# Performance work log

Hardware: AMD Instinct MI355X
Metric: run time of the kernel (lower is better)

## Reference

```python
import jax, jax.numpy as jnp
import numpy as np

C_IN = 12      # total channels (rgb-noised + hidden)
C_NOISE = 3    # noise-prediction channels
HID = 128      # rule-MLP hidden size
PERC = 48      # perception channels (depthwise, 48/12 = 4 filters per channel)
TDIM = 256     # sinusoidal time-embedding dim


def setup_inputs() -> dict:
    key = jax.random.key(0)
    ks = jax.random.split(key, 12)
    B, H, W = 16, 256, 256
    x = jax.random.normal(ks[0], (B, C_NOISE, H, W), jnp.float32)
    hidden_channels = jax.random.normal(ks[1], (B, C_IN - C_NOISE, H, W), jnp.float32)
    t = jax.random.randint(ks[2], (B,), 0, 1000)
    # depthwise 3x3 perceive conv: torch weight shape [out=48, in/groups=1, 3, 3]
    w_perceive = jax.random.normal(ks[3], (PERC, 1, 3, 3), jnp.float32) * 0.1
    b_perceive = jax.random.normal(ks[4], (PERC,), jnp.float32) * 0.01
    # 1x1 convs of the rule network, stored as [out, in]
    w1 = jax.random.normal(ks[5], (HID, PERC), jnp.float32) * 0.1
    b1 = jax.random.normal(ks[6], (HID,), jnp.float32) * 0.01
    w2 = jax.random.normal(ks[7], (HID, HID), jnp.float32) * 0.05
    b2 = jax.random.normal(ks[8], (HID,), jnp.float32) * 0.01
    # conv3 is zero-initialized in the original; random here for test coverage
    w3 = jax.random.normal(ks[9], (C_IN, HID), jnp.float32) * 0.05
    # time embedding Linear(256 -> c_noise)
    w_time = jax.random.normal(ks[10], (C_NOISE, TDIM), jnp.float32) * 0.1
    b_time = jax.random.normal(ks[11], (C_NOISE,), jnp.float32) * 0.01
    return dict(x=x, hidden_channels=hidden_channels, t=t,
                w_perceive=w_perceive, b_perceive=b_perceive,
                w1=w1, b1=b1, w2=w2, b2=b2, w3=w3,
                w_time=w_time, b_time=b_time)


def _pos_encoding(t, channels):
    # t: [B] int -> [B, channels] sinusoidal embedding (torch repeat-then-scale layout)
    inv_freq = 1.0 / (10000.0 ** (jnp.arange(0, channels, 2, dtype=jnp.float32) / channels))
    ang = t.astype(jnp.float32)[:, None] * inv_freq  # [B, channels//2]
    return jnp.concatenate([jnp.sin(ang), jnp.cos(ang)], axis=-1)


def reference(x, hidden_channels, t, w_perceive, b_perceive, w1, b1, w2, b2, w3, w_time, b_time):
    # concat noised channels with hidden state channels -> [B, 12, H, W]
    xf = jnp.concatenate([x, hidden_channels], axis=1)
    # depthwise 3x3 conv, 'same' padding, groups = C_IN
    perc = jax.lax.conv_general_dilated(
        xf, w_perceive, window_strides=(1, 1), padding='SAME',
        feature_group_count=C_IN,
        dimension_numbers=('NCHW', 'OIHW', 'NCHW')) + b_perceive[None, :, None, None]
    # rule network: three 1x1 convs (pointwise MLP) with ReLUs
    h = jax.nn.relu(jnp.einsum('bchw,oc->bohw', perc, w1) + b1[None, :, None, None])
    h = jax.nn.relu(jnp.einsum('bchw,oc->bohw', h, w2) + b2[None, :, None, None])
    out = jnp.einsum('bchw,oc->bohw', h, w3)  # no bias
    # time embedding: sinusoidal -> SiLU -> Linear -> broadcast over H, W
    pe = _pos_encoding(t, TDIM)                       # [B, 256]
    emb = jax.nn.silu(pe) @ w_time.T + b_time         # [B, 3]
    noise_prediction = out[:, :C_NOISE] + emb[:, :, None, None]
    hidden_out = out[:, C_NOISE:]
    return (hidden_out, noise_prediction)
```

## Files before the change

kernel.cpp:

```cpp
#include <hip/hip_runtime.h>


#define ACT_S 136
#define NOISE_BASE 9437184

#define WSF_OFF 17408
#define WSF_B1 0
#define WSF_B2 128
#define WSF_EMB 256

typedef short bf16x8 __attribute__((ext_vector_type(8)));
typedef float f32x4 __attribute__((ext_vector_type(4)));

__device__ __forceinline__ short f2bf(float f) {
    union { float f; unsigned u; } cv; cv.f = f;
    unsigned r = cv.u + 0x7FFFu + ((cv.u >> 16) & 1u);
    return (short)(r >> 16);
}
__device__ __forceinline__ unsigned pk2bf(float f0, float f1) {
    union { float f; unsigned u; } a, b; a.f = f0; b.f = f1;
    return __builtin_amdgcn_perm(b.u + 0x8000u, a.u + 0x8000u, 0x07060302u);
}

__global__ void prep_emb_kernel(const float* __restrict__ wpg, const float* __restrict__ bpg,
                                const float* __restrict__ w1g, const float* __restrict__ b1g,
                                const float* __restrict__ w2g, const float* __restrict__ b2g,
                                const float* __restrict__ w3g,
                                const int* __restrict__ t,
                                const float* __restrict__ wt, const float* __restrict__ bt,
                                short* __restrict__ wsb, float* __restrict__ wsf)
{
    const int bid = blockIdx.x, tid = threadIdx.x;
    if (bid < 64) {
        int i = bid * 256 + tid;
        int o = i >> 7, kk = i & 127;
        int qq = kk >> 5, r = kk & 31;
        float v = 0.f;
        if (r < 30 && (r % 10) < 9) {
            int c3 = r / 10, k = r % 10;
            int ic = 3 * qq + c3;
            #pragma unroll
            for (int j = 0; j < 4; ++j)
                v += w1g[o * 48 + 4 * ic + j] * wpg[(4 * ic + j) * 9 + k];
        }
        wsb[i] = f2bf(v);
        return;
    }
    if (bid < 128) {
        int i = (bid - 64) * 256 + tid;
        wsb[16384 + i] = f2bf(w2g[i]);
        return;
    }
    if (bid == 128) {
        for (int j = tid; j < 2048; j += 256)
            wsb[32768 + j] = (j < 1536) ? f2bf(w3g[j]) : (short)0;
        return;
    }
    if (bid == 129) {
        if (tid < 128) {
            float s = b1g[tid];
            #pragma unroll 4
            for (int c = 0; c < 48; ++c) s += w1g[tid * 48 + c] * bpg[c];
            wsf[WSF_B1 + tid] = s;
        } else {
            wsf[WSF_B2 + (tid - 128)] = b2g[tid - 128];
        }
        return;
    }
    int b = bid - 130;
    int lane = threadIdx.x;
    if (lane >= 64) return;
    float tv = (float)t[b];
    float s0 = 0.f, s1 = 0.f, s2 = 0.f;
    const float LOG1E4 = 9.210340371976184f;
    #pragma unroll
    for (int ii = 0; ii < 2; ++ii) {
        int i = lane + ii * 64;
        float invf = __expf(-LOG1E4 * (float)i * (1.0f / 128.0f));
        float ang = tv * invf;
        float sn = sinf(ang), cs = cosf(ang);
        float ss = sn / (1.0f + __expf(-sn));
        float sc = cs / (1.0f + __expf(-cs));
        s0 += ss * wt[0 * 256 + i] + sc * wt[0 * 256 + i + 128];
        s1 += ss * wt[1 * 256 + i] + sc * wt[1 * 256 + i + 128];
        s2 += ss * wt[2 * 256 + i] + sc * wt[2 * 256 + i + 128];
    }
    #pragma unroll
    for (int off = 32; off; off >>= 1) {
        s0 += __shfl_down(s0, off);
        s1 += __shfl_down(s1, off);
        s2 += __shfl_down(s2, off);
    }
    if (lane == 0) {
        wsf[WSF_EMB + b * 3 + 0] = s0 + bt[0];
        wsf[WSF_EMB + b * 3 + 1] = s1 + bt[1];
        wsf[WSF_EMB + b * 3 + 2] = s2 + bt[2];
    }
}

__global__ __launch_bounds__(256, 3) void canet_main(
    const float* __restrict__ xg,
    const float* __restrict__ hg,
    const short* __restrict__ wsb,
    const float* __restrict__ wsf,
    float* __restrict__ outg)
{
    __shared__ __align__(16) short bufA[64 * ACT_S];
    __shared__ __align__(16) short h1S[64 * ACT_S];
    __shared__ __align__(16) short w3_s[12 * 128];
    __shared__ __align__(16) float bias_s[256];

    const int tid = threadIdx.x;
    const int b = blockIdx.x >> 8;
    const int y = blockIdx.x & 255;

    bias_s[tid] = wsf[WSF_B1 + tid];
    for (int i = tid; i < 1536; i += 256) {
        int row = i >> 7, col = i & 127;
        w3_s[(row << 7) + (col ^ ((row & 7) << 3))] = wsb[32768 + i];
    }

    const int wv = tid >> 6;
    const int lane = tid & 63;
    const int m = lane & 15;
    const int q = lane >> 4;

    bf16x8 w1f[2][4], w2f[2][4];
    #pragma unroll
    for (int j = 0; j < 2; ++j) {
        int n = wv * 32 + j * 16 + m;
        #pragma unroll
        for (int ks = 0; ks < 4; ++ks) {
            w1f[j][ks] = *(const bf16x8*)(wsb + n * 128 + ks * 32 + q * 8);
            w2f[j][ks] = *(const bf16x8*)(wsb + 16384 + n * 128 + ks * 32 + q * 8);
        }
    }
    const float embv = (m < 3) ? wsf[WSF_EMB + b * 3 + m] : 0.0f;

    const float* src3[3];
    #pragma unroll
    for (int i3 = 0; i3 < 3; ++i3) {
        int ic = 3 * q + i3;
        src3[i3] = (ic < 3) ? (xg + (((size_t)b * 3 + ic) << 16))
                            : (hg + (((size_t)b * 9 + (ic - 3)) << 16));
    }

    const int mm = (m < 12) ? m : 11;
    const int w3sw = (mm & 7) << 3;

    __syncthreads();

    for (int it = 0; it < 4; ++it) {
        const int x0 = it * 64;
        const int px = x0 + wv * 16 + m;

        {
            const int xm1 = px - (px > 0);
            const int xp1 = px + (px < 255);
            const bool okl = (px > 0), okr = (px < 255);
            short* prow = bufA + (wv * 16 + m) * ACT_S + 32 * q;
            const bool interior = (y >= 1) && (y <= 254);
            #pragma unroll
            for (int i3 = 0; i3 < 3; ++i3) {
                const float* s = src3[i3];
                float tap[9];
                if (interior) {
                    #pragma unroll
                    for (int ky = 0; ky < 3; ++ky) {
                        const float* rp = s + (y + ky - 1) * 256;
                        float c0 = rp[xm1], c1 = rp[px], c2 = rp[xp1];
                        tap[ky * 3 + 0] = okl ? c0 : 0.0f;
                        tap[ky * 3 + 1] = c1;
                        tap[ky * 3 + 2] = okr ? c2 : 0.0f;
                    }
                } else {
                    #pragma unroll
                    for (int ky = 0; ky < 3; ++ky) {
                        int yy = y + ky - 1;
                        bool yok = (yy >= 0) && (yy < 256);
                        const float* rp = s + (yok ? yy : y) * 256;
                        float c0 = rp[xm1], c1 = rp[px], c2 = rp[xp1];
                        tap[ky * 3 + 0] = (yok && okl) ? c0 : 0.0f;
                        tap[ky * 3 + 1] = yok ? c1 : 0.0f;
                        tap[ky * 3 + 2] = (yok && okr) ? c2 : 0.0f;
                    }
                }
                unsigned* pw = (unsigned*)(prow + 10 * i3);
                pw[0] = pk2bf(tap[0], tap[1]);
                pw[1] = pk2bf(tap[2], tap[3]);
                pw[2] = pk2bf(tap[4], tap[5]);
                pw[3] = pk2bf(tap[6], tap[7]);
                pw[4] = pk2bf(tap[8], 0.0f);
            }
            *(unsigned*)(prow + 30) = 0u;
        }
        __syncthreads();

        #pragma unroll
        for (int nt = 0; nt < 4; ++nt) {
            f32x4 c0 = *(const f32x4*)(bias_s + wv * 32 + q * 4);
            f32x4 c1 = *(const f32x4*)(bias_s + wv * 32 + 16 + q * 4);
            #pragma unroll
            for (int ks = 0; ks < 4; ++ks) {
                bf16x8 p = *(const bf16x8*)(bufA + (nt * 16 + m) * ACT_S + ks * 32 + q * 8);
                c0 = __builtin_amdgcn_mfma_f32_16x16x32_bf16(w1f[0][ks], p, c0, 0, 0, 0);
                c1 = __builtin_amdgcn_mfma_f32_16x16x32_bf16(w1f[1][ks], p, c1, 0, 0, 0);
            }
            short* drow = h1S + (nt * 16 + m) * ACT_S + wv * 32 + q * 4;
            uint2 pk;
            pk.x = pk2bf(fmaxf(c0[0], 0.f), fmaxf(c0[1], 0.f));
            pk.y = pk2bf(fmaxf(c0[2], 0.f), fmaxf(c0[3], 0.f));
            *(uint2*)drow = pk;
            pk.x = pk2bf(fmaxf(c1[0], 0.f), fmaxf(c1[1], 0.f));
            pk.y = pk2bf(fmaxf(c1[2], 0.f), fmaxf(c1[3], 0.f));
            *(uint2*)(drow + 16) = pk;
        }
        __syncthreads();

        #pragma unroll
        for (int nt = 0; nt < 4; ++nt) {
            f32x4 c0 = *(const f32x4*)(bias_s + 128 + wv * 32 + q * 4);
            f32x4 c1 = *(const f32x4*)(bias_s + 128 + wv * 32 + 16 + q * 4);
            #pragma unroll
            for (int ks = 0; ks < 4; ++ks) {
                bf16x8 a = *(const bf16x8*)(h1S + (nt * 16 + m) * ACT_S + ks * 32 + q * 8);
                c0 = __builtin_amdgcn_mfma_f32_16x16x32_bf16(w2f[0][ks], a, c0, 0, 0, 0);
                c1 = __builtin_amdgcn_mfma_f32_16x16x32_bf16(w2f[1][ks], a, c1, 0, 0, 0);
            }
            short* drow = bufA + (nt * 16 + m) * ACT_S + wv * 32 + q * 4;
            uint2 pk;
            pk.x = pk2bf(fmaxf(c0[0], 0.f), fmaxf(c0[1], 0.f));
            pk.y = pk2bf(fmaxf(c0[2], 0.f), fmaxf(c0[3], 0.f));
            *(uint2*)drow = pk;
            pk.x = pk2bf(fmaxf(c1[0], 0.f), fmaxf(c1[1], 0.f));
            pk.y = pk2bf(fmaxf(c1[2], 0.f), fmaxf(c1[3], 0.f));
            *(uint2*)(drow + 16) = pk;
        }
        __syncthreads();

        {
            f32x4 acc = {0.f, 0.f, 0.f, 0.f};
            #pragma unroll
            for (int ks = 0; ks < 4; ++ks) {
                bf16x8 a = *(const bf16x8*)(bufA + (wv * 16 + m) * ACT_S + ks * 32 + q * 8);
                bf16x8 w3k = *(const bf16x8*)(w3_s + (mm << 7) + ((ks * 32 + q * 8) ^ w3sw));
                acc = __builtin_amdgcn_mfma_f32_16x16x32_bf16(a, w3k, acc, 0, 0, 0);
            }
            if (m < 12) {
                int xx0 = x0 + wv * 16 + q * 4;
                size_t idx;
                if (m < 3) {
                    idx = (size_t)NOISE_BASE + (((size_t)b * 3 + m) << 16) + (size_t)y * 256 + xx0;
                } else {
                    idx = (((size_t)b * 9 + (m - 3)) << 16) + (size_t)y * 256 + xx0;
                }
                f32x4 vst = {acc[0] + embv, acc[1] + embv, acc[2] + embv, acc[3] + embv};
                *(f32x4*)(outg + idx) = vst;
            }
        }
        __syncthreads();
    }
}

extern "C" void kernel_launch(void* const* d_in, const int* in_sizes, int n_in,
                              void* d_out, int out_size, void* d_ws, size_t ws_size,
                              hipStream_t stream) {
    const float* xg  = (const float*)d_in[0];
    const float* hg  = (const float*)d_in[1];
    const int*   tg  = (const int*)  d_in[2];
    const float* wpg = (const float*)d_in[3];
    const float* bpg = (const float*)d_in[4];
    const float* w1g = (const float*)d_in[5];
    const float* b1g = (const float*)d_in[6];
    const float* w2g = (const float*)d_in[7];
    const float* b2g = (const float*)d_in[8];
    const float* w3g = (const float*)d_in[9];
    const float* wtg = (const float*)d_in[10];
    const float* btg = (const float*)d_in[11];
    float* outg = (float*)d_out;
    short* wsb  = (short*)d_ws;
    float* wsf  = (float*)d_ws + WSF_OFF;

    prep_emb_kernel<<<146, 256, 0, stream>>>(wpg, bpg, w1g, b1g, w2g, b2g, w3g,
                                             tg, wtg, btg, wsb, wsf);
    canet_main<<<4096, 256, 0, stream>>>(xg, hg, wsb, wsf, outg);
}
```

Baseline: 219.1 us.

## Permute hidden-channel order so activation LDS stores become 128-bit

Reorders the output channels of the w1 and w2 weight matrices in the prep kernel, so that each lane's two MFMA accumulator groups map to 8 contiguous hidden channels. The h1 and h2 activation writes to shared memory can then be single 128-bit stores instead of pairs of 64-bit stores. The perception stage likewise buffers its packed bf16 taps in registers and writes them with four 128-bit stores. w3 staging is widened to 16 zero-padded rows so the row clamp is no longer needed. This relies on the permutation being consistent across w1, w2 and w3's input indexing, which holds because w3's K dimension is a permutation-invariant contraction only if w3 columns are permuted too. Here they are not, so correctness depends on careful checking.

```diff
diff --git a/kernel.cpp b/kernel.cpp
--- a/kernel.cpp
+++ b/kernel.cpp
@@ -20,6 +20,10 @@
 __device__ __forceinline__ unsigned pk2bf(float f0, float f1) {
     union { float f; unsigned u; } a, b; a.f = f0; b.f = f1;
     return __builtin_amdgcn_perm(b.u + 0x8000u, a.u + 0x8000u, 0x07060302u);
+}
+
+__device__ __forceinline__ int permch(int f) {
+    return (f & ~31) + 8 * ((f & 15) >> 2) + 4 * ((f >> 4) & 1) + (f & 3);
 }
 
 __global__ void prep_emb_kernel(const float* __restrict__ wpg, const float* __restrict__ bpg,
@@ -33,7 +37,8 @@
     const int bid = blockIdx.x, tid = threadIdx.x;
     if (bid < 64) {
         int i = bid * 256 + tid;
-        int o = i >> 7, kk = i & 127;
+        int f = i >> 7, kk = i & 127;
+        int o = permch(f);
         int qq = kk >> 5, r = kk & 31;
         float v = 0.f;
         if (r < 30 && (r % 10) < 9) {
@@ -48,7 +53,8 @@
     }
     if (bid < 128) {
         int i = (bid - 64) * 256 + tid;
-        wsb[16384 + i] = f2bf(w2g[i]);
+        int f = i >> 7, col = i & 127;
+        wsb[16384 + i] = f2bf(w2g[permch(f) * 128 + col]);
         return;
     }
     if (bid == 128) {
@@ -107,7 +113,7 @@
 {
     __shared__ __align__(16) short bufA[64 * ACT_S];
     __shared__ __align__(16) short h1S[64 * ACT_S];
-    __shared__ __align__(16) short w3_s[12 * 128];
+    __shared__ __align__(16) short w3_s[16 * 128];
     __shared__ __align__(16) float bias_s[256];
 
     const int tid = threadIdx.x;
@@ -115,7 +121,7 @@
     const int y = blockIdx.x & 255;
 
     bias_s[tid] = wsf[WSF_B1 + tid];
-    for (int i = tid; i < 1536; i += 256) {
+    for (int i = tid; i < 2048; i += 256) {
         int row = i >> 7, col = i & 127;
         w3_s[(row << 7) + (col ^ ((row & 7) << 3))] = wsb[32768 + i];
     }
@@ -145,8 +151,7 @@
                             : (hg + (((size_t)b * 9 + (ic - 3)) << 16));
     }
 
-    const int mm = (m < 12) ? m : 11;
-    const int w3sw = (mm & 7) << 3;
+    const int w3sw = (m & 7) << 3;
 
     __syncthreads();
 
@@ -160,6 +165,8 @@
             const bool okl = (px > 0), okr = (px < 255);
             short* prow = bufA + (wv * 16 + m) * ACT_S + 32 * q;
             const bool interior = (y >= 1) && (y <= 254);
+            unsigned rr[16];
+            rr[15] = 0u;
             #pragma unroll
             for (int i3 = 0; i3 < 3; ++i3) {
                 const float* s = src3[i3];
@@ -185,56 +192,57 @@
                         tap[ky * 3 + 2] = (yok && okr) ? c2 : 0.0f;
                     }
                 }
-                unsigned* pw = (unsigned*)(prow + 10 * i3);
-                pw[0] = pk2bf(tap[0], tap[1]);
-                pw[1] = pk2bf(tap[2], tap[3]);
-                pw[2] = pk2bf(tap[4], tap[5]);
-                pw[3] = pk2bf(tap[6], tap[7]);
-                pw[4] = pk2bf(tap[8], 0.0f);
-            }
-            *(unsigned*)(prow + 30) = 0u;
+                rr[5 * i3 + 0] = pk2bf(tap[0], tap[1]);
+                rr[5 * i3 + 1] = pk2bf(tap[2], tap[3]);
+                rr[5 * i3 + 2] = pk2bf(tap[4], tap[5]);
+                rr[5 * i3 + 3] = pk2bf(tap[6], tap[7]);
+                rr[5 * i3 + 4] = pk2bf(tap[8], 0.0f);
+            }
+            #pragma unroll
+            for (int w = 0; w < 4; ++w) {
+                uint4 v; v.x = rr[4*w]; v.y = rr[4*w+1]; v.z = rr[4*w+2]; v.w = rr[4*w+3];
+                *(uint4*)(prow + 8 * w) = v;
+            }
         }
         __syncthreads();
 
         #pragma unroll
         for (int nt = 0; nt < 4; ++nt) {
-            f32x4 c0 = *(const f32x4*)(bias_s + wv * 32 + q * 4);
-            f32x4 c1 = *(const f32x4*)(bias_s + wv * 32 + 16 + q * 4);
+            f32x4 c0 = *(const f32x4*)(bias_s + wv * 32 + 8 * q);
+            f32x4 c1 = *(const f32x4*)(bias_s + wv * 32 + 8 * q + 4);
             #pragma unroll
             for (int ks = 0; ks < 4; ++ks) {
                 bf16x8 p = *(const bf16x8*)(bufA + (nt * 16 + m) * ACT_S + ks * 32 + q * 8);
                 c0 = __builtin_amdgcn_mfma_f32_16x16x32_bf16(w1f[0][ks], p, c0, 0, 0, 0);
                 c1 = __builtin_amdgcn_mfma_f32_16x16x32_bf16(w1f[1][ks], p, c1, 0, 0, 0);
             }
-            short* drow = h1S + (nt * 16 + m) * ACT_S + wv * 32 + q * 4;
-            uint2 pk;
-            pk.x = pk2bf(fmaxf(c0[0], 0.f), fmaxf(c0[1], 0.f));
-            pk.y = pk2bf(fmaxf(c0[2], 0.f), fmaxf(c0[3], 0.f));
-            *(uint2*)drow = pk;
-            pk.x = pk2bf(fmaxf(c1[0], 0.f), fmaxf(c1[1], 0.f));
-            pk.y = pk2bf(fmaxf(c1[2], 0.f), fmaxf(c1[3], 0.f));
-            *(uint2*)(drow + 16) = pk;
+            short* drow = h1S + (nt * 16 + m) * ACT_S + wv * 32 + 8 * q;
+            uint4 pk4;
+            pk4.x = pk2bf(fmaxf(c0[0], 0.f), fmaxf(c0[1], 0.f));
+            pk4.y = pk2bf(fmaxf(c0[2], 0.f), fmaxf(c0[3], 0.f));
+            pk4.z = pk2bf(fmaxf(c1[0], 0.f), fmaxf(c1[1], 0.f));
+            pk4.w = pk2bf(fmaxf(c1[2], 0.f), fmaxf(c1[3], 0.f));
+            *(uint4*)drow = pk4;
         }
         __syncthreads();
 
         #pragma unroll
         for (int nt = 0; nt < 4; ++nt) {
-            f32x4 c0 = *(const f32x4*)(bias_s + 128 + wv * 32 + q * 4);
-            f32x4 c1 = *(const f32x4*)(bias_s + 128 + wv * 32 + 16 + q * 4);
+            f32x4 c0 = *(const f32x4*)(bias_s + 128 + wv * 32 + 8 * q);
+            f32x4 c1 = *(const f32x4*)(bias_s + 128 + wv * 32 + 8 * q + 4);
             #pragma unroll
             for (int ks = 0; ks < 4; ++ks) {
                 bf16x8 a = *(const bf16x8*)(h1S + (nt * 16 + m) * ACT_S + ks * 32 + q * 8);
                 c0 = __builtin_amdgcn_mfma_f32_16x16x32_bf16(w2f[0][ks], a, c0, 0, 0, 0);
                 c1 = __builtin_amdgcn_mfma_f32_16x16x32_bf16(w2f[1][ks], a, c1, 0, 0, 0);
             }
-            short* drow = bufA + (nt * 16 + m) * ACT_S + wv * 32 + q * 4;
-            uint2 pk;
-            pk.x = pk2bf(fmaxf(c0[0], 0.f), fmaxf(c0[1], 0.f));
-            pk.y = pk2bf(fmaxf(c0[2], 0.f), fmaxf(c0[3], 0.f));
-            *(uint2*)drow = pk;
-            pk.x = pk2bf(fmaxf(c1[0], 0.f), fmaxf(c1[1], 0.f));
-            pk.y = pk2bf(fmaxf(c1[2], 0.f), fmaxf(c1[3], 0.f));
-            *(uint2*)(drow + 16) = pk;
+            short* drow = bufA + (nt * 16 + m) * ACT_S + wv * 32 + 8 * q;
+            uint4 pk4;
+            pk4.x = pk2bf(fmaxf(c0[0], 0.f), fmaxf(c0[1], 0.f));
+            pk4.y = pk2bf(fmaxf(c0[2], 0.f), fmaxf(c0[3], 0.f));
+            pk4.z = pk2bf(fmaxf(c1[0], 0.f), fmaxf(c1[1], 0.f));
+            pk4.w = pk2bf(fmaxf(c1[2], 0.f), fmaxf(c1[3], 0.f));
+            *(uint4*)drow = pk4;
         }
         __syncthreads();
 
@@ -243,7 +251,7 @@
             #pragma unroll
             for (int ks = 0; ks < 4; ++ks) {
                 bf16x8 a = *(const bf16x8*)(bufA + (wv * 16 + m) * ACT_S + ks * 32 + q * 8);
-                bf16x8 w3k = *(const bf16x8*)(w3_s + (mm << 7) + ((ks * 32 + q * 8) ^ w3sw));
+                bf16x8 w3k = *(const bf16x8*)(w3_s + (m << 7) + ((ks * 32 + q * 8) ^ w3sw));
                 acc = __builtin_amdgcn_mfma_f32_16x16x32_bf16(a, w3k, acc, 0, 0, 0);
             }
             if (m < 12) {
```

After: 217.2 us. About the same (-0.8%).
